# Kernel tuning notes

Hardware: AMD Instinct MI355X
Metric: run time of the kernel (lower is better)

## Reference

```python
import jax, jax.numpy as jnp
import numpy as np

DIM = 32
B, H, W = 4, 256, 256


def conv1x1(x, w, b):
    # x: [B,C,H,W], w: [O,C], b: [O]
    return jnp.einsum('bchw,oc->bohw', x, w) + b[None, :, None, None]


def conv3x3(x, w, b):
    # x: [B,C,H,W], w: [O,C,3,3]
    out = jax.lax.conv_general_dilated(
        x, w, window_strides=(1, 1), padding='SAME',
        dimension_numbers=('NCHW', 'OIHW', 'NCHW'))
    return out + b[None, :, None, None]


def fft2d(x):
    # fft2 over last two dims, then fftshift over ALL dims (torch default)
    f = jnp.fft.fftshift(jnp.fft.fft2(x, norm='ortho'))
    return jnp.concatenate([f.real, f.imag], axis=1)  # [B,2C,H,W]


def ifft2d(x):
    f = jnp.fft.ifftshift(x)  # over ALL dims (torch default)
    re, im = jnp.split(f, 2, axis=1)
    c = jax.lax.complex(re, im)
    return jnp.abs(jnp.fft.ifft2(c, norm='ortho'))  # [B,C,H,W]


def setup_inputs() -> dict:
    key = jax.random.key(0)
    ks = jax.random.split(key, 16)
    C = DIM
    s = 0.02  # small init keeps the global-HW dot products in a sane softmax range
    inp = {
        'x': jax.random.normal(ks[0], (B, C, H, W), jnp.float32),
        'y': jax.random.normal(ks[1], (B, C, H, W), jnp.float32),
        'wq': jax.random.normal(ks[2], (C, C), jnp.float32) * s,
        'bq': jnp.zeros((C,), jnp.float32),
        'wk': jax.random.normal(ks[3], (C, C), jnp.float32) * s,
        'bk': jnp.zeros((C,), jnp.float32),
        'wv': jax.random.normal(ks[4], (C, C), jnp.float32) * s,
        'bv': jnp.zeros((C,), jnp.float32),
        'wd': jax.random.normal(ks[5], (C, C), jnp.float32) * s,
        'bd': jnp.zeros((C,), jnp.float32),
        'wc': jax.random.normal(ks[6], (2 * C, 2 * C, 3, 3), jnp.float32) * s,
        'bc': jnp.zeros((2 * C,), jnp.float32),
        'wi': jax.random.normal(ks[7], (2 * C, 2 * C, 3, 3), jnp.float32) * s,
        'bi': jnp.zeros((2 * C,), jnp.float32),
    }
    return inp


def reference(x, y, wq, bq, wk, bk, wv, bv, wd, bd, wc, bc, wi, bi):
    b, c, h, w = x.shape
    xq = conv1x1(x, wq, bq).reshape(b, c, h * w)            # [B,C,HW]
    dft = conv3x3(fft2d(conv1x1(y, wd, bd)), wc, bc)        # [B,2C,H,W]
    yk, yv = jnp.split(dft, 2, axis=1)
    yk = conv1x1(yk, wk, bk).reshape(b, c, h * w)
    yv = conv1x1(yv, wv, bv).reshape(b, c, h * w)
    att = jnp.einsum('bcn,bdn->bcd', xq, yk)                # [B,C,C]
    att = jax.nn.softmax(att, axis=1)                       # softmax over dim=1 (as in torch)
    out = jnp.einsum('bcd,bdn->bcn', att, yv).reshape(b, c, h, w)
    out = out + ifft2d(conv3x3(jax.nn.relu(dft), wi, bi))
    return out
```

## Files before the change

### kernel.cpp

```cpp
#include <hip/hip_runtime.h>
#include <math.h>

#define HW_ (256*256)
#define CH 32
#define CH2 64
#define BATCH 4

typedef short bf16x8 __attribute__((ext_vector_type(8)));
typedef float f32x4 __attribute__((ext_vector_type(4)));

__device__ __forceinline__ unsigned short f2bf(float f) {
    union { float f; unsigned u; } v; v.f = f;
    unsigned r = v.u + 0x7fffu + ((v.u >> 16) & 1u);
    return (unsigned short)(r >> 16);
}
__device__ __forceinline__ float bf2f(unsigned h) {
    union { unsigned u; float f; } v; v.u = h << 16;
    return v.f;
}

__device__ __forceinline__ int ctof_slot(int s) {
    return s < 16 ? s + 16 : s < 32 ? s + 32 : s < 48 ? s - 32 : s - 16;
}

__device__ __forceinline__ float2 cmul(float2 a, float2 b) {
    return make_float2(a.x*b.x - a.y*b.y, a.x*b.y + a.y*b.x);
}

__device__ __forceinline__ uint4 relu_bf16x8(uint4 v) {
    unsigned* pv = (unsigned*)&v;
    #pragma unroll
    for (int q = 0; q < 4; ++q) {
        unsigned a = pv[q];
        unsigned lo = a & 0xffffu, hi = a >> 16;
        if (lo & 0x8000u) lo = 0;
        if (hi & 0x8000u) hi = 0;
        pv[q] = lo | (hi << 16);
    }
    return v;
}

__device__ __forceinline__ void build_tw4(float2* tw, float sign) {
    int tid = threadIdx.x;
    float ang = sign * 6.2831853071795864769f * (float)tid / 256.0f;
    float s, c; sincosf(ang, &s, &c);
    tw[tid] = make_float2(c, s);
}

template<int SGN>
__device__ __forceinline__ void fft16_reg(float2* x, const float2* tw) {
    float2 u[16];
    #pragma unroll
    for (int m0 = 0; m0 < 4; ++m0) {
        float2 x0 = x[m0], x1 = x[m0+4], x2 = x[m0+8], x3 = x[m0+12];
        float2 t0 = make_float2(x0.x+x2.x, x0.y+x2.y);
        float2 t1 = make_float2(x0.x-x2.x, x0.y-x2.y);
        float2 t2 = make_float2(x1.x+x3.x, x1.y+x3.y);
        float2 t3 = make_float2(x1.x-x3.x, x1.y-x3.y);
        float2 r  = make_float2(-SGN*t3.y, SGN*t3.x);
        u[m0*4+0] = make_float2(t0.x+t2.x, t0.y+t2.y);
        u[m0*4+1] = make_float2(t1.x+r.x,  t1.y+r.y);
        u[m0*4+2] = make_float2(t0.x-t2.x, t0.y-t2.y);
        u[m0*4+3] = make_float2(t1.x-r.x,  t1.y-r.y);
    }
    #pragma unroll
    for (int m0 = 1; m0 < 4; ++m0)
        #pragma unroll
        for (int a = 1; a < 4; ++a)
            u[m0*4+a] = cmul(u[m0*4+a], tw[(16*m0*a) & 255]);
    #pragma unroll
    for (int a = 0; a < 4; ++a) {
        float2 x0 = u[a], x1 = u[4+a], x2 = u[8+a], x3 = u[12+a];
        float2 t0 = make_float2(x0.x+x2.x, x0.y+x2.y);
        float2 t1 = make_float2(x0.x-x2.x, x0.y-x2.y);
        float2 t2 = make_float2(x1.x+x3.x, x1.y+x3.y);
        float2 t3 = make_float2(x1.x-x3.x, x1.y-x3.y);
        float2 r  = make_float2(-SGN*t3.y, SGN*t3.x);
        x[a]    = make_float2(t0.x+t2.x, t0.y+t2.y);
        x[a+4]  = make_float2(t1.x+r.x,  t1.y+r.y);
        x[a+8]  = make_float2(t0.x-t2.x, t0.y-t2.y);
        x[a+12] = make_float2(t1.x-r.x,  t1.y-r.y);
    }
}

template<int SGN>
__device__ __forceinline__ void fft_core16(float2* A, const float2* tw) {
    const int tid = threadIdx.x;
    const int l = tid >> 4;
    const int d = tid & 15;
    const int base = l*257;
    float2 x[16];
    #pragma unroll
    for (int n1 = 0; n1 < 16; ++n1) x[n1] = A[base + n1*16 + d];
    fft16_reg<SGN>(x, tw);
    #pragma unroll
    for (int k0 = 1; k0 < 16; ++k0) x[k0] = cmul(x[k0], tw[d*k0]);
    #pragma unroll
    for (int k0 = 0; k0 < 16; ++k0) A[base + k0*16 + ((d + k0) & 15)] = x[k0];
    __syncthreads();
    #pragma unroll
    for (int n0 = 0; n0 < 16; ++n0) x[n0] = A[base + d*16 + ((n0 + d) & 15)];
    fft16_reg<SGN>(x, tw);
    #pragma unroll
    for (int k1 = 0; k1 < 16; ++k1) A[base + d + k1*16] = x[k1];
    __syncthreads();
}

__global__ __launch_bounds__(256) void k_fft_fwd1(const unsigned short* __restrict__ yd, ushort2* __restrict__ CAt) {
    __shared__ float2 A[16*257];
    __shared__ float2 tw[256];
    build_tw4(tw, -1.0f);
    int blk = blockIdx.x;
    int bp = blk >> 4, h0 = (blk & 15) << 4;
    int b = bp >> 4, p = bp & 15;
    const float sc = 1.0f/16.0f;
    const unsigned short* s0 = yd + ((size_t)(b*CH + 2*p))*HW_ + (size_t)h0*256;
    const unsigned short* s1 = s0 + HW_;
    for (int idx = threadIdx.x; idx < 16*64; idx += 256) {
        int l = idx >> 6, w4 = (idx & 63) << 2;
        uint2 va = *(const uint2*)(s0 + l*256 + w4);
        uint2 vb = *(const uint2*)(s1 + l*256 + w4);
        A[l*257 + w4+0] = make_float2(bf2f(va.x & 0xffffu)*sc, bf2f(vb.x & 0xffffu)*sc);
        A[l*257 + w4+1] = make_float2(bf2f(va.x >> 16)*sc, bf2f(vb.x >> 16)*sc);
        A[l*257 + w4+2] = make_float2(bf2f(va.y & 0xffffu)*sc, bf2f(vb.y & 0xffffu)*sc);
        A[l*257 + w4+3] = make_float2(bf2f(va.y >> 16)*sc, bf2f(vb.y >> 16)*sc);
    }
    __syncthreads();
    fft_core16<-1>(A, tw);
    int t = threadIdx.x;
    unsigned short pk[32];
    #pragma unroll
    for (int l = 0; l < 16; ++l) {
        float2 v = A[l*257 + t];
        pk[2*l]   = f2bf(v.x);
        pk[2*l+1] = f2bf(v.y);
    }
    uint4* d4 = (uint4*)(CAt + (size_t)bp*HW_ + (size_t)t*256 + h0);
    const uint4* s4 = (const uint4*)pk;
    d4[0] = s4[0]; d4[1] = s4[1]; d4[2] = s4[2]; d4[3] = s4[3];
}

__global__ __launch_bounds__(256) void k_fft_fwd2(const ushort2* __restrict__ CAt, unsigned short* __restrict__ FSH) {
    __shared__ float2 A[16*257];
    __shared__ float2 tw[256];
    build_tw4(tw, -1.0f);
    int blk = blockIdx.x;
    int b = blk >> 8, ph = (blk >> 7) & 1, vu = blk & 127;
    bool sp = (vu == 0);
    int col0 = vu, col1 = sp ? 128 : (256 - vu);
    const float sc = 1.0f/16.0f;
    for (int idx = threadIdx.x; idx < 16*256; idx += 256) {
        int l = idx >> 8, h = idx & 255;
        int p = l >> 1, s = l & 1;
        int col = s ? col1 : col0;
        ushort2 v = CAt[((size_t)(b*16 + ph*8 + p)*256 + col)*256 + h];
        A[l*257 + h] = make_float2(bf2f(v.x)*sc, bf2f(v.y)*sc);
    }
    __syncthreads();
    fft_core16<-1>(A, tw);
    int t = threadIdx.x;
    int bt = (b + 2) & 3;
    int ht = (t + 128) & 255;
    int tn = (256 - t) & 255;
    #pragma unroll
    for (int s = 0; s < 2; ++s) {
        int v = s ? col1 : col0;
        int wt = (v + 128) & 255;
        unsigned short pk[32];
        #pragma unroll
        for (int p = 0; p < 8; ++p) {
            int lA = 2*p + s;
            int lB = sp ? lA : (2*p + 1 - s);
            float2 Za = A[lA*257 + t];
            float2 Zb = A[lB*257 + tn];
            float xr = (Za.x + Zb.x)*0.5f, xi = (Za.y - Zb.y)*0.5f;
            float dr = Za.x - Zb.x,        di = Za.y + Zb.y;
            float yr = di*0.5f,            yi = -dr*0.5f;
            pk[2*p]     = f2bf(xr);
            pk[2*p+1]   = f2bf(yr);
            pk[16+2*p]  = f2bf(xi);
            pk[17+2*p]  = f2bf(yi);
        }
        unsigned short* dst = FSH + ((((size_t)bt*256 + ht)*256 + wt)*64 + ph*32);
        uint4* d4 = (uint4*)dst;
        const uint4* s4 = (const uint4*)pk;
        d4[0] = s4[0]; d4[1] = s4[1]; d4[2] = s4[2]; d4[3] = s4[3];
    }
}

__global__ __launch_bounds__(256) void k_conv1x1w(const float* __restrict__ in, const float* __restrict__ w,
                                                  const float* __restrict__ bias, unsigned short* __restrict__ out,
                                                  const float* __restrict__ wc, const float* __restrict__ wi,
                                                  unsigned short* __restrict__ d1, unsigned short* __restrict__ d2) {
    __shared__ float ts[32*257];
    int blk = blockIdx.x;
    int tid = threadIdx.x;
    if (blk >= 1024) {
        int i = (blk - 1024)*256 + tid;
        int half = i >= 36864;
        int j = i - half*36864;
        int tap = j >> 12, rem = j & 4095, oc = rem >> 6, s = rem & 63;
        if (half) {
            d2[j] = f2bf(wi[((size_t)(oc*64 + s))*9 + tap]);
        } else {
            int ic = ctof_slot(s);
            d1[j] = f2bf(wc[((size_t)(oc*64 + ic))*9 + tap]);
        }
        return;
    }
    int b = blk >> 8, h = blk & 255;
    const float* src = in + (size_t)b*CH*HW_ + (size_t)h*256;
    for (int idx = tid; idx < 32*256; idx += 256) {
        int c = idx >> 8, ww = idx & 255;
        ts[c*257 + ww] = src[(size_t)c*HW_ + ww];
    }
    __syncthreads();
    float acc[32];
    #pragma unroll
    for (int o = 0; o < 32; ++o) acc[o] = bias[o];
    for (int c = 0; c < 32; ++c) {
        float v = ts[c*257 + tid];
        #pragma unroll
        for (int o = 0; o < 32; ++o) acc[o] += w[o*32 + c] * v;
    }
    unsigned short* dst = out + (size_t)b*CH*HW_ + (size_t)h*256 + tid;
    #pragma unroll
    for (int o = 0; o < 32; ++o) dst[(size_t)o*HW_] = f2bf(acc[o]);
}

template<int MODE>
__global__ __launch_bounds__(256) void k_conv3(const unsigned short* __restrict__ in_cl,
                                               const unsigned short* __restrict__ wpk,
                                               const float* __restrict__ bias,
                                               unsigned short* __restrict__ outp) {
    __shared__ __align__(16) char Xs[2112*16];
    int tid = threadIdx.x;
    int blk = blockIdx.x;
    int wseg = blk & 3, hg = (blk >> 2) & 63, b = blk >> 8;
    int h0 = hg*4, w0 = wseg*64;

    int lane = tid & 63;
    int wv = tid >> 6;
    int l16 = lane & 15, lq = lane >> 4;

    for (int gl = tid; gl < 2112; gl += 256) {
        int slot = gl / 528;
        int rem  = gl - slot*528;
        int col  = rem >> 3, hseg = rem & 7;
        int hh = h0 - 1 + slot;
        int wcol = w0 - 1 + col;
        uint4 v = make_uint4(0,0,0,0);
        if (hh >= 0 && hh < 256 && wcol >= 0 && wcol < 256) {
            v = *(const uint4*)(in_cl + (((size_t)(b*256 + hh)*256 + wcol)*64) + hseg*8);
            if (MODE == 1) v = relu_bf16x8(v);
        }
        *(uint4*)(Xs + ((gl << 4) ^ ((col & 7) << 4))) = v;
    }

    const unsigned short* wb = wpk + ((size_t)((lane & 15) + ((tid & 32) ? 0 : 0)))*0;
    bf16x8 wcur[8], wnxt[8];
    #pragma unroll
    for (int q = 0; q < 8; ++q) {
        int oc = (q >> 1)*16 + l16;
        int hs = (q & 1)*4 + lq;
        wcur[q] = *(const bf16x8*)(wpk + oc*64 + hs*8);
    }
    __syncthreads();

    f32x4 acc[4][4];
    #pragma unroll
    for (int i = 0; i < 4; ++i)
        #pragma unroll
        for (int j = 0; j < 4; ++j) acc[i][j] = (f32x4)0.0f;

    uint4 xr0 = make_uint4(0,0,0,0), xr1 = make_uint4(0,0,0,0), xr2 = make_uint4(0,0,0,0);

    #pragma unroll
    for (int tap = 0; tap < 9; ++tap) {
        const int dy = tap / 3, dx = tap - dy*3;

        if (tap < 8) {
            #pragma unroll
            for (int q = 0; q < 8; ++q) {
                int oc = (q >> 1)*16 + l16;
                int hs = (q & 1)*4 + lq;
                wnxt[q] = *(const bf16x8*)(wpk + (size_t)(tap+1)*4096 + oc*64 + hs*8);
            }
        }
        if (dx == 0 && dy < 2) {
            int hh = h0 + dy + 3;
            bool hv = hh < 256;
            xr0 = make_uint4(0,0,0,0); xr1 = make_uint4(0,0,0,0); xr2 = make_uint4(0,0,0,0);
            {
                int gl = tid; int col = gl >> 3, hs = gl & 7;
                int wcol = w0 - 1 + col;
                if (hv && wcol >= 0 && wcol < 256)
                    xr0 = *(const uint4*)(in_cl + (((size_t)(b*256 + hh)*256 + wcol)*64) + hs*8);
            }
            {
                int gl = tid + 256; int col = gl >> 3, hs = gl & 7;
                int wcol = w0 - 1 + col;
                if (hv && wcol >= 0 && wcol < 256)
                    xr1 = *(const uint4*)(in_cl + (((size_t)(b*256 + hh)*256 + wcol)*64) + hs*8);
            }
            if (tid < 16) {
                int gl = tid + 512; int col = gl >> 3, hs = gl & 7;
                int wcol = w0 - 1 + col;
                if (hv && wcol < 256)
                    xr2 = *(const uint4*)(in_cl + (((size_t)(b*256 + hh)*256 + wcol)*64) + hs*8);
            }
        }

        int slot = (wv + dy) & 3;
        #pragma unroll
        for (int kk = 0; kk < 2; ++kk) {
            int hs = kk*4 + lq;
            bf16x8 xf[4];
            #pragma unroll
            for (int j = 0; j < 4; ++j) {
                int col = j*16 + l16 + dx;
                int g = slot*528 + col*8 + hs;
                xf[j] = *(const bf16x8*)(Xs + ((g << 4) ^ ((col & 7) << 4)));
            }
            #pragma unroll
            for (int i = 0; i < 4; ++i) {
                bf16x8 wf = wcur[i*2 + kk];
                #pragma unroll
                for (int j = 0; j < 4; ++j) {
                    if (MODE == 0)
                        acc[i][j] = __builtin_amdgcn_mfma_f32_16x16x32_bf16(wf, xf[j], acc[i][j], 0, 0, 0);
                    else
                        acc[i][j] = __builtin_amdgcn_mfma_f32_16x16x32_bf16(xf[j], wf, acc[i][j], 0, 0, 0);
                }
            }
        }

        if (dx == 2 && dy < 2) {
            __syncthreads();
            int slotn = dy & 3;
            {
                int gl = tid; int col = gl >> 3;
                uint4 v = (MODE == 1) ? relu_bf16x8(xr0) : xr0;
                int g = slotn*528 + gl;
                *(uint4*)(Xs + ((g << 4) ^ ((col & 7) << 4))) = v;
            }
            {
                int gl = tid + 256; int col = gl >> 3;
                uint4 v = (MODE == 1) ? relu_bf16x8(xr1) : xr1;
                int g = slotn*528 + gl;
                *(uint4*)(Xs + ((g << 4) ^ ((col & 7) << 4))) = v;
            }
            if (tid < 16) {
                int gl = tid + 512; int col = gl >> 3;
                uint4 v = (MODE == 1) ? relu_bf16x8(xr2) : xr2;
                int g = slotn*528 + gl;
                *(uint4*)(Xs + ((g << 4) ^ ((col & 7) << 4))) = v;
            }
            __syncthreads();
        }

        if (tap < 8) {
            #pragma unroll
            for (int q = 0; q < 8; ++q) wcur[q] = wnxt[q];
        }
    }

    int h = h0 + wv;
    if (MODE == 0) {
        #pragma unroll
        for (int j = 0; j < 4; ++j) {
            int px = w0 + j*16 + l16;
            unsigned short* orow = outp + (((size_t)b*256 + h)*256 + px)*64;
            #pragma unroll
            for (int i = 0; i < 4; ++i) {
                int oc0 = i*16 + lq*4;
                float4 bv = *(const float4*)(bias + oc0);
                unsigned short c0 = f2bf(acc[i][j][0] + bv.x);
                unsigned short c1 = f2bf(acc[i][j][1] + bv.y);
                unsigned short c2 = f2bf(acc[i][j][2] + bv.z);
                unsigned short c3 = f2bf(acc[i][j][3] + bv.w);
                uint2 u;
                u.x = (unsigned)c0 | ((unsigned)c1 << 16);
                u.y = (unsigned)c2 | ((unsigned)c3 << 16);
                *(uint2*)(orow + oc0) = u;
            }
        }
    } else {
        #pragma unroll
        for (int i = 0; i < 4; ++i) {
            int oc = i*16 + l16;
            float bv = bias[oc];
            unsigned short* oplane = outp + ((size_t)b*64 + oc)*HW_ + (size_t)h*256;
            #pragma unroll
            for (int j = 0; j < 4; ++j) {
                int px0 = w0 + j*16 + lq*4;
                unsigned short c0 = f2bf(acc[i][j][0] + bv);
                unsigned short c1 = f2bf(acc[i][j][1] + bv);
                unsigned short c2 = f2bf(acc[i][j][2] + bv);
                unsigned short c3 = f2bf(acc[i][j][3] + bv);
                uint2 u;
                u.x = (unsigned)c0 | ((unsigned)c1 << 16);
                u.y = (unsigned)c2 | ((unsigned)c3 << 16);
                *(uint2*)(oplane + px0) = u;
            }
        }
    }
}

__global__ __launch_bounds__(256) void k_gram(const float* __restrict__ x, const unsigned short* __restrict__ dcl,
                                              float* __restrict__ Mpart, float* __restrict__ Sxp, float* __restrict__ Sdp) {
    __shared__ __align__(16) float xs[32*132];
    __shared__ __align__(16) unsigned short dst_[32*136];
    __shared__ float mred[1024];
    __shared__ float sxred[32];
    __shared__ float sdred[32];
    int blk = blockIdx.x;
    int b = blk >> 7, chunk = blk & 127;
    int tid = threadIdx.x, lane = tid & 63, wv = tid >> 6;
    int l16 = lane & 15, lq = lane >> 4;
    for (int idx = tid; idx < 1024; idx += 256) mred[idx] = 0.0f;
    if (tid < 32) { sxred[tid] = 0.0f; sdred[tid] = 0.0f; }

    const float* xb = x + (size_t)b*CH*HW_;
    const unsigned short* db = dcl + (size_t)b*HW_*64;

    f32x4 acc[2][2];
    #pragma unroll
    for (int i = 0; i < 2; ++i)
        #pragma unroll
        for (int j = 0; j < 2; ++j) acc[i][j] = (f32x4)0.0f;
    float sx0 = 0, sx1 = 0, sd0 = 0, sd1 = 0;

    for (int q4 = 0; q4 < 4; ++q4) {
        int px0 = chunk*512 + q4*128;
        __syncthreads();
        #pragma unroll
        for (int p = 0; p < 4; ++p) {
            int g = tid + p*256;
            int c = g >> 5, k4 = (g & 31) << 2;
            *(float4*)&xs[c*132 + k4] = *(const float4*)(xb + (size_t)c*HW_ + px0 + k4);
        }
        #pragma unroll
        for (int p = 0; p < 2; ++p) {
            int g = tid + p*256;
            int px = g >> 2, quad = g & 3;
            uint4 v = *(const uint4*)(db + (size_t)(px0 + px)*64 + quad*8);
            const unsigned short* pv = (const unsigned short*)&v;
            #pragma unroll
            for (int u = 0; u < 8; ++u) dst_[(quad*8 + u)*136 + px] = pv[u];
        }
        __syncthreads();
        #pragma unroll
        for (int ks = 0; ks < 4; ++ks) {
            int k0 = ks*32 + lq*8;
            float4 xa = *(const float4*)&xs[l16*132 + k0];
            float4 xc = *(const float4*)&xs[l16*132 + k0 + 4];
            float4 ya = *(const float4*)&xs[(16+l16)*132 + k0];
            float4 yc = *(const float4*)&xs[(16+l16)*132 + k0 + 4];
            bf16x8 a0, a1;
            const float* pxa = (const float*)&xa;
            const float* pxc = (const float*)&xc;
            const float* pya = (const float*)&ya;
            const float* pyc = (const float*)&yc;
            #pragma unroll
            for (int j = 0; j < 4; ++j) {
                a0[j]   = (short)f2bf(pxa[j]);  sx0 += pxa[j];
                a0[4+j] = (short)f2bf(pxc[j]);  sx0 += pxc[j];
                a1[j]   = (short)f2bf(pya[j]);  sx1 += pya[j];
                a1[4+j] = (short)f2bf(pyc[j]);  sx1 += pyc[j];
            }
            bf16x8 b0 = *(const bf16x8*)&dst_[l16*136 + k0];
            bf16x8 b1 = *(const bf16x8*)&dst_[(16+l16)*136 + k0];
            #pragma unroll
            for (int j = 0; j < 8; ++j) {
                sd0 += bf2f((unsigned short)b0[j]);
                sd1 += bf2f((unsigned short)b1[j]);
            }
            acc[0][0] = __builtin_amdgcn_mfma_f32_16x16x32_bf16(a0, b0, acc[0][0], 0, 0, 0);
            acc[0][1] = __builtin_amdgcn_mfma_f32_16x16x32_bf16(a0, b1, acc[0][1], 0, 0, 0);
            acc[1][0] = __builtin_amdgcn_mfma_f32_16x16x32_bf16(a1, b0, acc[1][0], 0, 0, 0);
            acc[1][1] = __builtin_amdgcn_mfma_f32_16x16x32_bf16(a1, b1, acc[1][1], 0, 0, 0);
        }
    }
    __syncthreads();

    #pragma unroll
    for (int fi = 0; fi < 2; ++fi)
        #pragma unroll
        for (int fj = 0; fj < 2; ++fj)
            #pragma unroll
            for (int r = 0; r < 4; ++r)
                atomicAdd(&mred[(fi*16 + lq*4 + r)*32 + fj*16 + l16], acc[fi][fj][r]);

    sx0 += __shfl_xor(sx0, 16); sx0 += __shfl_xor(sx0, 32);
    sx1 += __shfl_xor(sx1, 16); sx1 += __shfl_xor(sx1, 32);
    sd0 += __shfl_xor(sd0, 16); sd0 += __shfl_xor(sd0, 32);
    sd1 += __shfl_xor(sd1, 16); sd1 += __shfl_xor(sd1, 32);
    if (lane < 16) {
        atomicAdd(&sxred[l16], sx0);
        atomicAdd(&sxred[l16 + 16], sx1);
        atomicAdd(&sdred[l16], sd0);
        atomicAdd(&sdred[l16 + 16], sd1);
    }
    __syncthreads();

    float* mp = Mpart + ((size_t)(b*128 + chunk))*1024;
    for (int idx = tid; idx < 1024; idx += 256) mp[idx] = mred[idx];
    if (tid < 32) {
        Sxp[(b*128 + chunk)*32 + tid] = sxred[tid];
        Sdp[(b*128 + chunk)*32 + tid] = sdred[tid];
    }
}

__global__ __launch_bounds__(256) void k_att(const float* __restrict__ Mpart, const float* __restrict__ Sxp,
                                              const float* __restrict__ Sdp,
                                              const float* __restrict__ wq, const float* __restrict__ bq,
                                              const float* __restrict__ wk, const float* __restrict__ bk,
                                              const float* __restrict__ wv, const float* __restrict__ bv,
                                              float* __restrict__ att2, float* __restrict__ sout) {
    __shared__ float Mls[1024], T1[1024], attls[32*33];
    __shared__ float wqs[1024], wks[1024], wvs[1024];
    __shared__ float q1[32], k1[32], sxs[32], sds[32];
    int tid = threadIdx.x;
    int b = blockIdx.x;
    for (int idx = tid; idx < 1024; idx += 256) { wqs[idx] = wq[idx]; wks[idx] = wk[idx]; wvs[idx] = wv[idx]; }
    #pragma unroll
    for (int q = 0; q < 4; ++q) {
        int o = tid + q*256;
        float s = 0;
        for (int c = 0; c < 128; ++c) s += Mpart[((size_t)(b*128 + c))*1024 + o];
        Mls[o] = s;
    }
    if (tid < 32) { float s = 0; for (int c = 0; c < 128; ++c) s += Sxp[(b*128 + c)*32 + tid]; sxs[tid] = s; }
    else if (tid < 64) { int e = tid - 32; float s = 0; for (int c = 0; c < 128; ++c) s += Sdp[(b*128 + c)*32 + e]; sds[e] = s; }
    __syncthreads();
    if (tid < 32) { float s=0; for (int a=0;a<32;++a) s += wqs[tid*32+a]*sxs[a]; q1[tid]=s; }
    else if (tid < 64) { int d=tid-32; float s=0; for (int e=0;e<32;++e) s += wks[d*32+e]*sds[e]; k1[d]=s; }
    for (int idx = tid; idx < 1024; idx += 256) {
        int c = idx >> 5, e = idx & 31;
        float s = 0;
        for (int a=0;a<32;++a) s += wqs[c*32+a]*Mls[a*32+e];
        T1[idx] = s;
    }
    __syncthreads();
    for (int idx = tid; idx < 1024; idx += 256) {
        int c = idx >> 5, d = idx & 31;
        float s = 0;
        for (int e=0;e<32;++e) s += T1[c*32+e]*wks[d*32+e];
        s += bq[c]*k1[d] + bk[d]*q1[c] + 65536.0f*bq[c]*bk[d];
        attls[c*33+d] = s;
    }
    __syncthreads();
    if (tid < 32) {
        int d = tid;
        float mx = -1e30f;
        for (int c=0;c<32;++c) mx = fmaxf(mx, attls[c*33+d]);
        float sum = 0;
        for (int c=0;c<32;++c) { float e_ = expf(attls[c*33+d]-mx); attls[c*33+d]=e_; sum+=e_; }
        float inv = 1.0f/sum;
        for (int c=0;c<32;++c) attls[c*33+d] *= inv;
    }
    __syncthreads();
    for (int idx = tid; idx < 1024; idx += 256) {
        int c = idx >> 5, e = idx & 31;
        float s = 0;
        for (int d=0; d<32; ++d) s += attls[c*33+d]*wvs[d*32+e];
        att2[b*1024 + idx] = s;
    }
    if (tid < 32) {
        float s=0; for (int d=0;d<32;++d) s += attls[tid*33+d]*bv[d];
        sout[b*32+tid] = s;
    }
}

__global__ __launch_bounds__(256) void k_fft_inv1(const unsigned short* __restrict__ G, ushort2* __restrict__ Z1T) {
    __shared__ float2 A[16*257];
    __shared__ float2 tw[256];
    build_tw4(tw, 1.0f);
    int blk = blockIdx.x;
    int bc = blk >> 4, w0 = (blk & 15) << 4;
    int b = bc >> 5, c = bc & 31;
    int bs = (b + 2) & 3;
    const float sc = 1.0f/16.0f;
    const unsigned short* gre = G + ((size_t)(bs*CH2 + c + 32))*HW_;
    const unsigned short* gim = G + ((size_t)(bs*CH2 + c))*HW_;
    for (int idx = threadIdx.x; idx < 16*256; idx += 256) {
        int h = idx >> 4, l = idx & 15;
        int hs = (h + 128) & 255;
        int ws = (w0 + l + 128) & 255;
        A[l*257 + h] = make_float2(bf2f(gre[(size_t)hs*256 + ws])*sc, bf2f(gim[(size_t)hs*256 + ws])*sc);
    }
    __syncthreads();
    fft_core16<1>(A, tw);
    ushort2* dst = Z1T + (size_t)bc*HW_;
    for (int idx = threadIdx.x; idx < 16*256; idx += 256) {
        int l = idx >> 8, h = idx & 255;
        float2 v = A[l*257 + h];
        dst[(size_t)(w0 + l)*256 + h] = make_ushort2(f2bf(v.x), f2bf(v.y));
    }
}

__global__ __launch_bounds__(256) void k_fft_inv2(const ushort2* __restrict__ Z1T, unsigned short* __restrict__ Mag) {
    __shared__ float2 A[16*257];
    __shared__ float2 tw[256];
    build_tw4(tw, 1.0f);
    int blk = blockIdx.x;
    int bc = blk >> 4, h0 = (blk & 15) << 4;
    const float sc = 1.0f/16.0f;
    const ushort2* src = Z1T + (size_t)bc*HW_ + h0;
    for (int idx = threadIdx.x; idx < 16*256; idx += 256) {
        int w = idx >> 4, l = idx & 15;
        ushort2 v = src[(size_t)w*256 + l];
        A[l*257 + w] = make_float2(bf2f(v.x)*sc, bf2f(v.y)*sc);
    }
    __syncthreads();
    fft_core16<1>(A, tw);
    unsigned short* dst = Mag + (size_t)bc*HW_ + (size_t)h0*256;
    for (int idx = threadIdx.x; idx < 16*256; idx += 256) {
        int l = idx >> 8, w = idx & 255;
        float2 v = A[l*257 + w];
        dst[l*256 + w] = f2bf(sqrtf(v.x*v.x + v.y*v.y));
    }
}

__global__ __launch_bounds__(256) void k_out(const unsigned short* __restrict__ dcl, const float* __restrict__ att2,
                                             const float* __restrict__ sv, const unsigned short* __restrict__ Mag,
                                             float* __restrict__ out) {
    __shared__ __align__(16) float A2ls[1024];
    __shared__ float svls[32];
    int blk = blockIdx.x; int b = blk >> 8, h = blk & 255;
    int tid = threadIdx.x;
    for (int idx = tid; idx < 1024; idx += 256) A2ls[idx] = att2[b*1024 + idx];
    if (tid < 32) svls[tid] = sv[b*32 + tid];
    __syncthreads();
    int px = tid;
    const uint4* dvp = (const uint4*)(dcl + ((((size_t)b*256 + h)*256 + px)*64 + 32));
    uint4 d0 = dvp[0], d1 = dvp[1];
    unsigned u[8] = {d0.x, d0.y, d0.z, d0.w, d1.x, d1.y, d1.z, d1.w};
    float dv[32];
    #pragma unroll
    for (int i = 0; i < 8; ++i) {
        dv[2*i]   = bf2f(u[i] & 0xffffu);
        dv[2*i+1] = bf2f(u[i] >> 16);
    }
    float accv[32];
    #pragma unroll
    for (int c = 0; c < 32; ++c) accv[c] = svls[c];
    #pragma unroll
    for (int q = 0; q < 8; ++q) {
        #pragma unroll
        for (int c = 0; c < 32; ++c) {
            float4 a4 = *(const float4*)&A2ls[c*32 + q*4];
            accv[c] += a4.x*dv[q*4] + a4.y*dv[q*4+1] + a4.z*dv[q*4+2] + a4.w*dv[q*4+3];
        }
    }
    const unsigned short* mb = Mag + (size_t)b*CH*HW_ + (size_t)h*256 + px;
    float* ob = out + (size_t)b*CH*HW_ + (size_t)h*256 + px;
    #pragma unroll
    for (int c = 0; c < 32; ++c) ob[(size_t)c*HW_] = accv[c] + bf2f(mb[(size_t)c*HW_]);
}

extern "C" void kernel_launch(void* const* d_in, const int* in_sizes, int n_in,
                              void* d_out, int out_size, void* d_ws, size_t ws_size,
                              hipStream_t stream) {
    const float* x  = (const float*)d_in[0];
    const float* y  = (const float*)d_in[1];
    const float* wq = (const float*)d_in[2];
    const float* bq = (const float*)d_in[3];
    const float* wk = (const float*)d_in[4];
    const float* bk = (const float*)d_in[5];
    const float* wv = (const float*)d_in[6];
    const float* bv = (const float*)d_in[7];
    const float* wd = (const float*)d_in[8];
    const float* bd = (const float*)d_in[9];
    const float* wc = (const float*)d_in[10];
    const float* bc = (const float*)d_in[11];
    const float* wi = (const float*)d_in[12];
    const float* bi = (const float*)d_in[13];
    float* out = (float*)d_out;

    char* ws = (char*)d_ws;
    size_t o = 0;
    unsigned short* R1   = (unsigned short*)(ws + o); o += (size_t)BATCH*CH*HW_*2;
    ushort2*        CAt  = (ushort2*)(ws + o);        o += (size_t)BATCH*CH*HW_*4;
    unsigned short* FSHc = (unsigned short*)(ws + o); o += (size_t)BATCH*CH2*HW_*2;
    unsigned short* DFTc = (unsigned short*)(ws + o); o += (size_t)BATCH*CH2*HW_*2;
    unsigned short* Gpl  = (unsigned short*)(ws + o); o += (size_t)BATCH*CH2*HW_*2;
    unsigned short* wpk1 = (unsigned short*)(ws + o); o += 9*64*64*2;
    unsigned short* wpk2 = (unsigned short*)(ws + o); o += 9*64*64*2;
    float*          Mpart= (float*)(ws + o);          o += (size_t)512*1024*4;
    float*          Sxp  = (float*)(ws + o);          o += 512*32*4;
    float*          Sdp  = (float*)(ws + o);          o += 512*32*4;
    float*          A2b  = (float*)(ws + o);          o += 4096*4;
    float*          Svb  = (float*)(ws + o);          o += 128*4;
    if (ws_size < o) return;

    ushort2*        Z1T = CAt;
    unsigned short* Mag = R1;

    k_conv1x1w<<<1312, 256, 0, stream>>>(y, wd, bd, R1, wc, wi, wpk1, wpk2);
    k_fft_fwd1<<<1024, 256, 0, stream>>>(R1, CAt);
    k_fft_fwd2<<<1024, 256, 0, stream>>>(CAt, FSHc);
    k_conv3<0><<<1024, 256, 0, stream>>>(FSHc, wpk1, bc, DFTc);
    k_conv3<1><<<1024, 256, 0, stream>>>(DFTc, wpk2, bi, Gpl);
    k_gram<<<512, 256, 0, stream>>>(x, DFTc, Mpart, Sxp, Sdp);
    k_att<<<4, 256, 0, stream>>>(Mpart, Sxp, Sdp, wq, bq, wk, bk, wv, bv, A2b, Svb);
    k_fft_inv1<<<2048, 256, 0, stream>>>(Gpl, Z1T);
    k_fft_inv2<<<2048, 256, 0, stream>>>(Z1T, Mag);
    k_out<<<1024, 256, 0, stream>>>(DFTc, A2b, Svb, Mag, out);
}
```

Measured before the change: 291.6 us.

## Stage conv3x3 weights in LDS per row and vectorize inverse FFT loads

The 3x3 conv kernel now stages each kernel row's weights (three taps) in swizzled shared memory, prefetched alongside the next input row. Previously every wave read per-tap weight fragments directly from global memory into registers. The intent is to cut redundant global weight traffic and free registers, at the cost of extra LDS reads per MFMA group and more shared memory per block. Separately, the inverse FFT stage kernels now load input with 16-byte vector loads per thread instead of scalar strided loads.

```diff
diff --git a/kernel.cpp b/kernel.cpp
--- a/kernel.cpp
+++ b/kernel.cpp
@@ -234,14 +234,13 @@
                                                const float* __restrict__ bias,
                                                unsigned short* __restrict__ outp) {
     __shared__ __align__(16) char Xs[2112*16];
+    __shared__ __align__(16) char Ws[1536*16];
     int tid = threadIdx.x;
     int blk = blockIdx.x;
     int wseg = blk & 3, hg = (blk >> 2) & 63, b = blk >> 8;
     int h0 = hg*4, w0 = wseg*64;
 
-    int lane = tid & 63;
-    int wv = tid >> 6;
-    int l16 = lane & 15, lq = lane >> 4;
+    const uint4* wsrc = (const uint4*)wpk;
 
     for (int gl = tid; gl < 2112; gl += 256) {
         int slot = gl / 528;
@@ -256,16 +255,17 @@
         }
         *(uint4*)(Xs + ((gl << 4) ^ ((col & 7) << 4))) = v;
     }
-
-    const unsigned short* wb = wpk + ((size_t)((lane & 15) + ((tid & 32) ? 0 : 0)))*0;
-    bf16x8 wcur[8], wnxt[8];
-    #pragma unroll
-    for (int q = 0; q < 8; ++q) {
-        int oc = (q >> 1)*16 + l16;
-        int hs = (q & 1)*4 + lq;
-        wcur[q] = *(const bf16x8*)(wpk + oc*64 + hs*8);
-    }
-    __syncthreads();
+    #pragma unroll
+    for (int q = 0; q < 6; ++q) {
+        int gw = tid + q*256;
+        int oc = (gw >> 3) & 63;
+        *(uint4*)(Ws + ((gw << 4) ^ ((oc & 7) << 4))) = wsrc[gw];
+    }
+    __syncthreads();
+
+    int lane = tid & 63;
+    int wv = tid >> 6;
+    int l16 = lane & 15, lq = lane >> 4;
 
     f32x4 acc[4][4];
     #pragma unroll
@@ -273,95 +273,98 @@
         #pragma unroll
         for (int j = 0; j < 4; ++j) acc[i][j] = (f32x4)0.0f;
 
-    uint4 xr0 = make_uint4(0,0,0,0), xr1 = make_uint4(0,0,0,0), xr2 = make_uint4(0,0,0,0);
-
-    #pragma unroll
-    for (int tap = 0; tap < 9; ++tap) {
-        const int dy = tap / 3, dx = tap - dy*3;
-
-        if (tap < 8) {
-            #pragma unroll
-            for (int q = 0; q < 8; ++q) {
-                int oc = (q >> 1)*16 + l16;
-                int hs = (q & 1)*4 + lq;
-                wnxt[q] = *(const bf16x8*)(wpk + (size_t)(tap+1)*4096 + oc*64 + hs*8);
-            }
-        }
-        if (dx == 0 && dy < 2) {
+    for (int dy = 0; dy < 3; ++dy) {
+        uint4 xr0 = make_uint4(0,0,0,0), xr1 = make_uint4(0,0,0,0), xr2 = make_uint4(0,0,0,0);
+        uint4 wr[6];
+        if (dy < 2) {
             int hh = h0 + dy + 3;
             bool hv = hh < 256;
-            xr0 = make_uint4(0,0,0,0); xr1 = make_uint4(0,0,0,0); xr2 = make_uint4(0,0,0,0);
             {
-                int gl = tid; int col = gl >> 3, hs = gl & 7;
+                int gl = tid;
+                int col = gl >> 3, hseg = gl & 7;
                 int wcol = w0 - 1 + col;
                 if (hv && wcol >= 0 && wcol < 256)
-                    xr0 = *(const uint4*)(in_cl + (((size_t)(b*256 + hh)*256 + wcol)*64) + hs*8);
+                    xr0 = *(const uint4*)(in_cl + (((size_t)(b*256 + hh)*256 + wcol)*64) + hseg*8);
             }
             {
-                int gl = tid + 256; int col = gl >> 3, hs = gl & 7;
+                int gl = tid + 256;
+                int col = gl >> 3, hseg = gl & 7;
                 int wcol = w0 - 1 + col;
                 if (hv && wcol >= 0 && wcol < 256)
-                    xr1 = *(const uint4*)(in_cl + (((size_t)(b*256 + hh)*256 + wcol)*64) + hs*8);
+                    xr1 = *(const uint4*)(in_cl + (((size_t)(b*256 + hh)*256 + wcol)*64) + hseg*8);
             }
             if (tid < 16) {
-                int gl = tid + 512; int col = gl >> 3, hs = gl & 7;
+                int gl = tid + 512;
+                int col = gl >> 3, hseg = gl & 7;
                 int wcol = w0 - 1 + col;
                 if (hv && wcol < 256)
-                    xr2 = *(const uint4*)(in_cl + (((size_t)(b*256 + hh)*256 + wcol)*64) + hs*8);
-            }
+                    xr2 = *(const uint4*)(in_cl + (((size_t)(b*256 + hh)*256 + wcol)*64) + hseg*8);
+            }
+            #pragma unroll
+            for (int q = 0; q < 6; ++q)
+                wr[q] = wsrc[(dy+1)*1536 + tid + q*256];
         }
 
         int slot = (wv + dy) & 3;
         #pragma unroll
-        for (int kk = 0; kk < 2; ++kk) {
-            int hs = kk*4 + lq;
-            bf16x8 xf[4];
-            #pragma unroll
-            for (int j = 0; j < 4; ++j) {
-                int col = j*16 + l16 + dx;
-                int g = slot*528 + col*8 + hs;
-                xf[j] = *(const bf16x8*)(Xs + ((g << 4) ^ ((col & 7) << 4)));
-            }
-            #pragma unroll
-            for (int i = 0; i < 4; ++i) {
-                bf16x8 wf = wcur[i*2 + kk];
+        for (int dx = 0; dx < 3; ++dx) {
+            #pragma unroll
+            for (int kk = 0; kk < 2; ++kk) {
+                int hseg = kk*4 + lq;
+                bf16x8 xf[4], wf[4];
                 #pragma unroll
                 for (int j = 0; j < 4; ++j) {
-                    if (MODE == 0)
-                        acc[i][j] = __builtin_amdgcn_mfma_f32_16x16x32_bf16(wf, xf[j], acc[i][j], 0, 0, 0);
-                    else
-                        acc[i][j] = __builtin_amdgcn_mfma_f32_16x16x32_bf16(xf[j], wf, acc[i][j], 0, 0, 0);
+                    int col = j*16 + l16 + dx;
+                    int g = slot*528 + col*8 + hseg;
+                    xf[j] = *(const bf16x8*)(Xs + ((g << 4) ^ ((col & 7) << 4)));
                 }
-            }
-        }
-
-        if (dx == 2 && dy < 2) {
+                #pragma unroll
+                for (int i = 0; i < 4; ++i) {
+                    int oc = i*16 + l16;
+                    int lw = dx*512 + oc*8 + hseg;
+                    wf[i] = *(const bf16x8*)(Ws + ((lw << 4) ^ ((oc & 7) << 4)));
+                    #pragma unroll
+                    for (int j = 0; j < 4; ++j) {
+                        if (MODE == 0)
+                            acc[i][j] = __builtin_amdgcn_mfma_f32_16x16x32_bf16(wf[i], xf[j], acc[i][j], 0, 0, 0);
+                        else
+                            acc[i][j] = __builtin_amdgcn_mfma_f32_16x16x32_bf16(xf[j], wf[i], acc[i][j], 0, 0, 0);
+                    }
+                }
+            }
+        }
+
+        if (dy < 2) {
             __syncthreads();
             int slotn = dy & 3;
             {
-                int gl = tid; int col = gl >> 3;
+                int gl = tid;
+                int col = gl >> 3;
                 uint4 v = (MODE == 1) ? relu_bf16x8(xr0) : xr0;
                 int g = slotn*528 + gl;
                 *(uint4*)(Xs + ((g << 4) ^ ((col & 7) << 4))) = v;
             }
             {
-                int gl = tid + 256; int col = gl >> 3;
+                int gl = tid + 256;
+                int col = gl >> 3;
                 uint4 v = (MODE == 1) ? relu_bf16x8(xr1) : xr1;
                 int g = slotn*528 + gl;
                 *(uint4*)(Xs + ((g << 4) ^ ((col & 7) << 4))) = v;
             }
             if (tid < 16) {
-                int gl = tid + 512; int col = gl >> 3;
+                int gl = tid + 512;
+                int col = gl >> 3;
                 uint4 v = (MODE == 1) ? relu_bf16x8(xr2) : xr2;
                 int g = slotn*528 + gl;
                 *(uint4*)(Xs + ((g << 4) ^ ((col & 7) << 4))) = v;
             }
+            #pragma unroll
+            for (int q = 0; q < 6; ++q) {
+                int gw = tid + q*256;
+                int oc = (gw >> 3) & 63;
+                *(uint4*)(Ws + ((gw << 4) ^ ((oc & 7) << 4))) = wr[q];
+            }
             __syncthreads();
-        }
-
-        if (tap < 8) {
-            #pragma unroll
-            for (int q = 0; q < 8; ++q) wcur[q] = wnxt[q];
         }
     }
 
@@ -584,11 +587,20 @@
     const float sc = 1.0f/16.0f;
     const unsigned short* gre = G + ((size_t)(bs*CH2 + c + 32))*HW_;
     const unsigned short* gim = G + ((size_t)(bs*CH2 + c))*HW_;
-    for (int idx = threadIdx.x; idx < 16*256; idx += 256) {
-        int h = idx >> 4, l = idx & 15;
+    {
+        int h = threadIdx.x;
         int hs = (h + 128) & 255;
-        int ws = (w0 + l + 128) & 255;
-        A[l*257 + h] = make_float2(bf2f(gre[(size_t)hs*256 + ws])*sc, bf2f(gim[(size_t)hs*256 + ws])*sc);
+        int wsb = (w0 + 128) & 255;
+        const uint4* pr = (const uint4*)(gre + (size_t)hs*256 + wsb);
+        const uint4* pi = (const uint4*)(gim + (size_t)hs*256 + wsb);
+        uint4 r0 = pr[0], r1 = pr[1];
+        uint4 i0 = pi[0], i1 = pi[1];
+        unsigned short re[16], im[16];
+        *(uint4*)&re[0] = r0; *(uint4*)&re[8] = r1;
+        *(uint4*)&im[0] = i0; *(uint4*)&im[8] = i1;
+        #pragma unroll
+        for (int l = 0; l < 16; ++l)
+            A[l*257 + h] = make_float2(bf2f(re[l])*sc, bf2f(im[l])*sc);
     }
     __syncthreads();
     fft_core16<1>(A, tw);
@@ -607,11 +619,16 @@
     int blk = blockIdx.x;
     int bc = blk >> 4, h0 = (blk & 15) << 4;
     const float sc = 1.0f/16.0f;
-    const ushort2* src = Z1T + (size_t)bc*HW_ + h0;
-    for (int idx = threadIdx.x; idx < 16*256; idx += 256) {
-        int w = idx >> 4, l = idx & 15;
-        ushort2 v = src[(size_t)w*256 + l];
-        A[l*257 + w] = make_float2(bf2f(v.x)*sc, bf2f(v.y)*sc);
+    {
+        int w = threadIdx.x;
+        const uint4* src = (const uint4*)(Z1T + (size_t)bc*HW_ + (size_t)w*256 + h0);
+        uint4 t0 = src[0], t1 = src[1], t2 = src[2], t3 = src[3];
+        ushort2 vv[16];
+        *(uint4*)&vv[0]  = t0; *(uint4*)&vv[4]  = t1;
+        *(uint4*)&vv[8]  = t2; *(uint4*)&vv[12] = t3;
+        #pragma unroll
+        for (int l = 0; l < 16; ++l)
+            A[l*257 + w] = make_float2(bf2f(vv[l].x)*sc, bf2f(vv[l].y)*sc);
     }
     __syncthreads();
     fft_core16<1>(A, tw);
```

Measured after the change: 271.0 us. 1.08x faster.
